# Performance work log

Hardware: AMD Instinct MI355X
Metric: run time of the kernel (lower is better)

Reference implementation:

```python
import jax, jax.numpy as jnp
import numpy as np

N, H_DIM, LATENT, MLP_H, F_OUT = 256, 128, 128, 256, 16
SUPP = 0.5  # ancestor_suppression_strength
EPS = 1e-12


def setup_inputs() -> dict:
    key = jax.random.key(0)
    ks = jax.random.split(key, 12)
    def w(k, shape):
        fan_in = shape[0]
        return jax.random.normal(k, shape, jnp.float32) / np.sqrt(fan_in)
    return {
        'z': jax.random.normal(ks[0], (LATENT,), jnp.float32),
        'targets': jax.random.randint(ks[1], (N, N), 0, 2, jnp.int32),
        'pos_emb': jax.random.normal(ks[2], (N, H_DIM), jnp.float32),
        'Ws1': w(ks[3], (H_DIM, H_DIM)),
        'Wn1': w(ks[4], (H_DIM, H_DIM)),
        'b1': jnp.zeros((H_DIM,), jnp.float32),
        'Ws2': w(ks[5], (H_DIM, H_DIM)),
        'Wn2': w(ks[6], (H_DIM, H_DIM)),
        'b2': jnp.zeros((H_DIM,), jnp.float32),
        'Wm1': w(ks[7], (LATENT + 3 * H_DIM, MLP_H)),
        'bm1': jnp.zeros((MLP_H,), jnp.float32),
        'Wm2': w(ks[8], (MLP_H, 1)),
        'bm2': jnp.zeros((1,), jnp.float32),
        'Wf': w(ks[9], (H_DIM, F_OUT)),
        'bf': jnp.zeros((F_OUT,), jnp.float32),
    }


def reference(z, targets, pos_emb, Ws1, Wn1, b1, Ws2, Wn2, b2,
              Wm1, bm1, Wm2, bm2, Wf, bf):
    tgt = jnp.tril(targets.astype(jnp.float32), -1)  # [N,N] strict lower: row=child, col=parent
    idx = jnp.arange(N)
    h0 = z  # decoder_init=None => hidden state init is z itself
    layers = ((Ws1, Wn1, b1), (Ws2, Wn2, b2))

    def gnn(Hs, M, active):
        # M[dst, src]: messages aggregated over incoming (parent) edges
        for Ws, Wn, b in layers:
            Hs = jax.nn.relu(Hs @ Ws + (M @ Hs) @ Wn + b) * active[:, None]
        return Hs

    def step(carry, t):
        Hs, anc, lp = carry
        Hs = Hs.at[t].set(h0 + pos_emb[t])          # new node t
        active = (idx <= t).astype(jnp.float32)
        M = tgt * (idx < t)[:, None].astype(jnp.float32)  # edges added in steps < t
        Hs = gnn(Hs, M, active)
        h_t = Hs[t]
        cand = (idx < t).astype(jnp.float32)        # candidate parents i < t
        mlp_in = jnp.concatenate([
            jnp.broadcast_to(h_t, (N, H_DIM)), Hs,
            jnp.broadcast_to(z, (N, LATENT)),
            jnp.broadcast_to(pos_emb[t], (N, H_DIM))], axis=1)
        logits = (jax.nn.relu(mlp_in @ Wm1 + bm1) @ Wm2 + bm2)[:, 0]
        probs = jax.nn.sigmoid(logits)
        # suppression[i] = prod_{j<t} (1 - s * anc[j][i])
        supp = jnp.prod(jnp.where((idx < t)[:, None], 1.0 - SUPP * anc, 1.0), axis=0)
        adj = probs * supp
        gt = tgt[t]
        logp = gt * jnp.log(adj + EPS) + (1.0 - gt) * jnp.log(1.0 - adj + EPS)
        lp = lp + jnp.sum(logp * cand)
        # ancestors of t = union over parents p of (anc[p] | {p})
        anc_t = jnp.minimum(1.0, gt @ anc + gt)
        anc = anc.at[t].set(anc_t)
        return (Hs, anc, lp), None

    H0 = jnp.zeros((N, H_DIM), jnp.float32).at[0].set(h0)
    anc0 = jnp.zeros((N, N), jnp.float32)
    (Hs, anc, lp), _ = jax.lax.scan(step, (H0, anc0, jnp.float32(0.0)), jnp.arange(1, N))
    # node_feature_decoder path: one more GNN pass over the full graph
    Hs = gnn(Hs, tgt, jnp.ones((N,), jnp.float32))
    X_out = Hs @ Wf + bf
    return tgt, X_out, lp
```

## Files before the change

### kernel.cpp

```cpp
#include <hip/hip_runtime.h>

#define NN 256
#define HD 128
#define GNN_NB 64
#define MLP_NB 64
#define NBLK 128
#define NTHR 512
#define D_HS 3
#define D_H1 2

#define HS_OFF 0
#define H1R_OFF 98304
#define PROG_OFF 163840
#define MF_OFF   (163840 + 2048)

#define STH_L 0
#define STM_L 512
#define PT_L  1024
#define TGT_L 0
#define PTM_L 2048
#define PT3_L 10240
#define HC_L  11264
#define CT_L  11776
#define CZ_L  12032
#define W2_L  12288
#define HP_L  12544
#define PART_L 12800
#define ANC_L 13312
#define LP_L  13344
#define LDS_FLOATS 13360

__device__ __forceinline__ float2 ldc_f2(const float* p) {
    unsigned long long u = __hip_atomic_load((const unsigned long long*)p,
                                             __ATOMIC_RELAXED, __HIP_MEMORY_SCOPE_AGENT);
    float2 r;
    r.x = __uint_as_float((unsigned)u);
    r.y = __uint_as_float((unsigned)(u >> 32));
    return r;
}
__device__ __forceinline__ void stc_f(float* p, float v) {
    __hip_atomic_store((unsigned*)p, __float_as_uint(v),
                       __ATOMIC_RELAXED, __HIP_MEMORY_SCOPE_AGENT);
}
__device__ __forceinline__ unsigned ldf(const unsigned* p) {
    return __hip_atomic_load(p, __ATOMIC_RELAXED, __HIP_MEMORY_SCOPE_AGENT);
}
__device__ __forceinline__ void stf(unsigned* p, unsigned v) {
    __hip_atomic_store(p, v, __ATOMIC_RELAXED, __HIP_MEMORY_SCOPE_AGENT);
}

__device__ __forceinline__ void bar_lds() {
    asm volatile("s_waitcnt lgkmcnt(0)\n\ts_barrier" ::: "memory");
}

__device__ __forceinline__ void wait_gnn(const unsigned* prog, const unsigned* mf,
                                         int b, unsigned dataTh, unsigned ringTh, int mlpTh)
{
    const int tid = threadIdx.x;
    if (tid < GNN_NB) {
        const unsigned th = (tid < b) ? dataTh : ringTh;
        if (th)
            while (ldf(prog + tid * 32) < th) __builtin_amdgcn_s_sleep(1);
    } else if (tid < 2 * GNN_NB) {
        if (mlpTh > 0)
            while ((int)ldf(mf + (tid - GNN_NB) * 32) < mlpTh) __builtin_amdgcn_s_sleep(1);
    }
    __syncthreads();
    asm volatile("" ::: "memory");
}

#define ISS(i) \
    float2 va##i, vb##i, vc##i, vd##i; \
    if ((i) < nst) { \
        const float* p_ = gsrc + (i) * 32 * HD; \
        if ((un >> (4 * (i)    )) & 1u) va##i = ldc_f2(p_); \
        if ((un >> (4 * (i) + 1)) & 1u) vb##i = ldc_f2(p_ + HD); \
        if ((un >> (4 * (i) + 2)) & 1u) vc##i = ldc_f2(p_ + 2 * HD); \
        if ((un >> (4 * (i) + 3)) & 1u) vd##i = ldc_f2(p_ + 3 * HD); \
    }
#define ACCP(v, b) { \
    const float f0_ = (float)((s0 >> (b)) & 1u); \
    const float f1_ = (float)((s1 >> (b)) & 1u); \
    const float f2_ = (float)((s2 >> (b)) & 1u); \
    const float f3_ = (float)((s3 >> (b)) & 1u); \
    m0.x = fmaf(f0_, v.x, m0.x); m0.y = fmaf(f0_, v.y, m0.y); \
    m1.x = fmaf(f1_, v.x, m1.x); m1.y = fmaf(f1_, v.y, m1.y); \
    m2.x = fmaf(f2_, v.x, m2.x); m2.y = fmaf(f2_, v.y, m2.y); \
    m3.x = fmaf(f3_, v.x, m3.x); m3.y = fmaf(f3_, v.y, m3.y); }
#define ACC1(v, b) if ((un >> (b)) & 1u) { ACCP(v, b) }
#define CNS(i) if ((i) < nst) { ACC1(va##i, 4*(i)) ACC1(vb##i, 4*(i)+1) \
                                ACC1(vc##i, 4*(i)+2) ACC1(vd##i, 4*(i)+3) }

__device__ __forceinline__ void layer(const float* src, float* dst, const float* bias,
    const float* z, const float* pos_emb, float* lds,
    const float2 (&wsA)[16], const float2 (&wnA)[16],
    unsigned mk0, unsigned mk1, unsigned mk2, unsigned mk3,
    int R0, int rmax, int tgate, int tnew, int lane, int wv, int tid)
{
    const int rmaxblk = min(rmax, R0 + 3);
    const int nst = (rmaxblk + 31) >> 5;
    const unsigned s0 = (R0     < tgate) ? mk0 : 0u;
    const unsigned s1 = (R0 + 1 < tgate) ? mk1 : 0u;
    const unsigned s2 = (R0 + 2 < tgate) ? mk2 : 0u;
    const unsigned s3 = (R0 + 3 < tgate) ? mk3 : 0u;
    const unsigned un = s0 | s1 | s2 | s3;

    if (tnew >= R0 && tnew < R0 + 4) {
        const int dr = tnew - R0;
        if (tid < HD) lds[STH_L + dr * HD + tid] = z[tid] + pos_emb[tnew * HD + tid];
    }

    const float* gsrc = src + wv * 4 * HD + 2 * lane;
    float2 m0 = make_float2(0.f, 0.f), m1 = m0, m2 = m0, m3 = m0;
    ISS(0) ISS(1) ISS(2) ISS(3) ISS(4) ISS(5) ISS(6) ISS(7)
    CNS(0) CNS(1) CNS(2) CNS(3) CNS(4) CNS(5) CNS(6) CNS(7)

    float* pt = lds + PT_L + (wv * 4) * HD + 2 * lane;
    *(float2*)pt = m0; *(float2*)(pt + HD) = m1;
    *(float2*)(pt + 2 * HD) = m2; *(float2*)(pt + 3 * HD) = m3;
    bar_lds();
    {
        const int dr = tid >> 7, k = tid & 127;
        float s = 0.f;
#pragma unroll
        for (int w = 0; w < 8; ++w) s += lds[PT_L + (w * 4 + dr) * HD + k];
        lds[STM_L + dr * HD + k] = s;
    }
    bar_lds();
    const int ks = wv * 16;
    float2 a0 = make_float2(0.f, 0.f), a1 = a0, a2 = a0, a3 = a0;
#define MV(dr, areg) { \
    const float4 hp = *(const float4*)(lds + STH_L + (dr) * HD + ks + 4 * kq); \
    const float4 mp = *(const float4*)(lds + STM_L + (dr) * HD + ks + 4 * kq); \
    areg.x = fmaf(hp.x, wsA[4*kq].x,   fmaf(mp.x, wnA[4*kq].x,   areg.x)); \
    areg.y = fmaf(hp.x, wsA[4*kq].y,   fmaf(mp.x, wnA[4*kq].y,   areg.y)); \
    areg.x = fmaf(hp.y, wsA[4*kq+1].x, fmaf(mp.y, wnA[4*kq+1].x, areg.x)); \
    areg.y = fmaf(hp.y, wsA[4*kq+1].y, fmaf(mp.y, wnA[4*kq+1].y, areg.y)); \
    areg.x = fmaf(hp.z, wsA[4*kq+2].x, fmaf(mp.z, wnA[4*kq+2].x, areg.x)); \
    areg.y = fmaf(hp.z, wsA[4*kq+2].y, fmaf(mp.z, wnA[4*kq+2].y, areg.y)); \
    areg.x = fmaf(hp.w, wsA[4*kq+3].x, fmaf(mp.w, wnA[4*kq+3].x, areg.x)); \
    areg.y = fmaf(hp.w, wsA[4*kq+3].y, fmaf(mp.w, wnA[4*kq+3].y, areg.y)); }
#pragma unroll
    for (int kq = 0; kq < 4; ++kq) { MV(0, a0) MV(1, a1) MV(2, a2) MV(3, a3) }
#undef MV
    *(float2*)pt = a0; *(float2*)(pt + HD) = a1;
    *(float2*)(pt + 2 * HD) = a2; *(float2*)(pt + 3 * HD) = a3;
    bar_lds();
    {
        const int dr = tid >> 7, c = tid & 127;
        float o = bias[c];
#pragma unroll
        for (int w = 0; w < 8; ++w) o += lds[PT_L + (w * 4 + dr) * HD + c];
        o = fmaxf(o, 0.f);
        lds[STH_L + dr * HD + c] = o;
        const int R = R0 + dr;
        if (R <= rmaxblk) stc_f(dst + R * HD + c, o);
    }
}

__device__ __forceinline__ void ct_calc(const float* hsP, const float* pos_emb,
                                        const float* Wm1, float* lds, int s)
{
    const int tid = threadIdx.x;
    if (tid < 64) {
        const float2 v = ldc_f2(hsP + s * HD + 2 * tid);
        lds[HP_L + 2 * tid] = v.x; lds[HP_L + 2 * tid + 1] = v.y;
    } else if (tid < 128) {
        const int l2 = tid - 64;
        lds[HP_L + 128 + 2 * l2]     = pos_emb[s * HD + 2 * l2];
        lds[HP_L + 128 + 2 * l2 + 1] = pos_emb[s * HD + 2 * l2 + 1];
    }
    __syncthreads();
    const int c = tid & 255, half = tid >> 8;
    float acc = 0.f;
    const float* w = half ? (Wm1 + 384 * 256 + c) : (Wm1 + c);
    const float* hh = lds + HP_L + half * 128;
#pragma unroll 4
    for (int k = 0; k < HD; ++k) acc = fmaf(hh[k], w[k * 256], acc);
    lds[PART_L + half * 256 + c] = acc;
    __syncthreads();
    if (tid < 256)
        lds[CT_L + tid] = lds[CZ_L + tid] + lds[PART_L + tid] + lds[PART_L + 256 + tid];
}

__device__ __forceinline__ void mlp_step(const float* hsP, const float* bm2,
                                         const float4 (&wm)[16], float* lds, int mb, int s)
{
    const int tid = threadIdx.x, lane = tid & 63, wv = tid >> 6;
    const int ks = wv * 16;
    if (wv < 4) {
        const int i = 4 * mb + wv;
        float2 v = make_float2(0.f, 0.f);
        if (i < s) v = ldc_f2(hsP + i * HD + 2 * lane);
        *(float2*)(lds + HC_L + wv * HD + 2 * lane) = v;
    }
    __syncthreads();
    float4 a0 = make_float4(0.f, 0.f, 0.f, 0.f), a1 = a0, a2 = a0, a3 = a0;
#pragma unroll
    for (int kk = 0; kk < 16; ++kk) {
        const int k = ks + kk;
        const float h0 = lds[HC_L + 0 * HD + k];
        const float h1 = lds[HC_L + 1 * HD + k];
        const float h2 = lds[HC_L + 2 * HD + k];
        const float h3 = lds[HC_L + 3 * HD + k];
        const float4 w = wm[kk];
        a0.x = fmaf(h0, w.x, a0.x); a0.y = fmaf(h0, w.y, a0.y);
        a0.z = fmaf(h0, w.z, a0.z); a0.w = fmaf(h0, w.w, a0.w);
        a1.x = fmaf(h1, w.x, a1.x); a1.y = fmaf(h1, w.y, a1.y);
        a1.z = fmaf(h1, w.z, a1.z); a1.w = fmaf(h1, w.w, a1.w);
        a2.x = fmaf(h2, w.x, a2.x); a2.y = fmaf(h2, w.y, a2.y);
        a2.z = fmaf(h2, w.z, a2.z); a2.w = fmaf(h2, w.w, a2.w);
        a3.x = fmaf(h3, w.x, a3.x); a3.y = fmaf(h3, w.y, a3.y);
        a3.z = fmaf(h3, w.z, a3.z); a3.w = fmaf(h3, w.w, a3.w);
    }
    *(float4*)(lds + PTM_L + (wv * 4 + 0) * 256 + 4 * lane) = a0;
    *(float4*)(lds + PTM_L + (wv * 4 + 1) * 256 + 4 * lane) = a1;
    *(float4*)(lds + PTM_L + (wv * 4 + 2) * 256 + 4 * lane) = a2;
    *(float4*)(lds + PTM_L + (wv * 4 + 3) * 256 + 4 * lane) = a3;
    __syncthreads();
    {
        const int c = tid & 255, ci2 = (tid >> 8) * 2;
#pragma unroll
        for (int q = 0; q < 2; ++q) {
            const int ci = ci2 + q;
            float v = lds[CT_L + c];
#pragma unroll
            for (int w = 0; w < 8; ++w) v += lds[PTM_L + (w * 4 + ci) * 256 + c];
            lds[PT3_L + ci * 256 + c] = fmaxf(v, 0.f) * lds[W2_L + c];
        }
    }
    __syncthreads();
    if (wv < 4) {
        const int ci = wv, i = 4 * mb + ci;
        if (i < s) {
            float sd = lds[PT3_L + ci * 256 + lane] + lds[PT3_L + ci * 256 + 64 + lane]
                     + lds[PT3_L + ci * 256 + 128 + lane] + lds[PT3_L + ci * 256 + 192 + lane];
#pragma unroll
            for (int off = 32; off > 0; off >>= 1) sd += __shfl_xor(sd, off);
            if (lane == 0) {
                const unsigned* gtl = (const unsigned*)(lds + TGT_L) + s * 8;
                unsigned* ancl = (unsigned*)(lds + ANC_L);
                const float logit = sd + bm2[0];
                const float prob = 1.f / (1.f + expf(-logit));
                unsigned cnt = 0, has = 0;
#pragma unroll
                for (int w = 0; w < 8; ++w) {
                    const unsigned av = ancl[ci * 8 + w];
                    cnt += __popc(av);
                    has |= av & gtl[w];
                }
                const float supp = ldexpf(1.f, -(int)cnt);
                const float adj = prob * supp;
                const unsigned gt = (gtl[i >> 5] >> (i & 31)) & 1u;
                const float lpv = gt ? logf(adj + 1e-12f) : logf(1.f - adj + 1e-12f);
                atomicAdd((float*)(lds + LP_L), lpv);
                if (has | gt) ancl[ci * 8 + (s >> 5)] |= (1u << (s & 31));
            }
        }
    }
}

extern "C" __global__ void __launch_bounds__(NTHR, 2)
fused_gnn(const float* z, const int* targets, const float* pos_emb,
          const float* Ws1, const float* Wn1, const float* b1,
          const float* Ws2, const float* Wn2, const float* b2,
          const float* Wm1, const float* bm1, const float* Wm2, const float* bm2,
          const float* Wf, const float* bf, float* out, float* ws)
{
    __shared__ __align__(16) float lds[LDS_FLOATS];
    const int b = blockIdx.x;
    const int tid = threadIdx.x, lane = tid & 63, wv = tid >> 6;

    unsigned* prog = (unsigned*)(ws + PROG_OFF);
    unsigned* mf   = (unsigned*)(ws + MF_OFF);
    float* lp_out = out + NN * NN + NN * 16;
    const int ks = wv * 16;

    if (b < GNN_NB) {
        const int R0 = b * 4;
        float2 ws1[16], wn1[16], ws2[16], wn2[16];
#pragma unroll
        for (int kk = 0; kk < 16; ++kk) {
            ws1[kk] = *(const float2*)(Ws1 + (ks + kk) * HD + 2 * lane);
            wn1[kk] = *(const float2*)(Wn1 + (ks + kk) * HD + 2 * lane);
            ws2[kk] = *(const float2*)(Ws2 + (ks + kk) * HD + 2 * lane);
            wn2[kk] = *(const float2*)(Wn2 + (ks + kk) * HD + 2 * lane);
        }
        unsigned mk0, mk1, mk2, mk3;
        {
            const int srcl = (lane < 32) ? (((lane >> 2) << 5) + wv * 4 + (lane & 3)) : 0;
#define BALLOT_MK(dr, dst) { \
            const int r_ = R0 + (dr); \
            const bool p_ = (lane < 32) && (srcl < r_) && (targets[r_ * NN + srcl] != 0); \
            const unsigned long long bm_ = __ballot(p_); \
            dst = (unsigned)__builtin_amdgcn_readfirstlane((int)(unsigned)bm_); }
            BALLOT_MK(0, mk0) BALLOT_MK(1, mk1) BALLOT_MK(2, mk2) BALLOT_MK(3, mk3)
#undef BALLOT_MK
        }
        lds[STH_L + tid] = (b == 0 && tid < HD) ? z[tid] : 0.f;
        {
            const int dr = tid >> 7, c = tid & 127, r = R0 + dr;
            stc_f(ws + HS_OFF + r * HD + c, (r == 0) ? z[c] : 0.f);
        }
        if (wv < 4) {
            const int r = R0 + wv;
            const int4 tv = ((const int4*)(targets + r * NN))[lane];
            float4 ov;
            ov.x = (4 * lane     < r) ? (float)tv.x : 0.f;
            ov.y = (4 * lane + 1 < r) ? (float)tv.y : 0.f;
            ov.z = (4 * lane + 2 < r) ? (float)tv.z : 0.f;
            ov.w = (4 * lane + 3 < r) ? (float)tv.w : 0.f;
            ((float4*)(out + r * NN))[lane] = ov;
        }
        __syncthreads();
        if (tid == 0) stf(prog + b * 32, 1u);

        for (int t = 1; t <= 256; ++t) {
            const float* hsP = ws + HS_OFF + ((t - 1) % D_HS) * 32768;
            float* h1c = ws + H1R_OFF + (t & 1) * 32768;
            float* hsN = ws + HS_OFF + (t % D_HS) * 32768;
            const int rmax  = (t <= 255) ? t : 255;
            const int tgate = (t <= 255) ? t : 300;
            const int tnew  = (t <= 255) ? t : -1;
            const bool act = (R0 <= rmax);

            if (act) {
                wait_gnn(prog, mf, b, 2u * t - 1u,
                         (t > D_H1) ? (2u * (t - D_H1) + 1u) : 0u, 0);
                layer(hsP, h1c, b1, z, pos_emb, lds, ws1, wn1,
                      mk0, mk1, mk2, mk3, R0, rmax, tgate, tnew, lane, wv, tid);
            }
            __syncthreads();
            if (tid == 0) stf(prog + b * 32, 2u * t);

            if (act) {
                wait_gnn(prog, mf, b, 2u * t,
                         (t > D_HS) ? (2u * (t - D_HS + 1)) : 0u, t - D_HS);
                layer(h1c, hsN, b2, z, pos_emb, lds, ws2, wn2,
                      mk0, mk1, mk2, mk3, R0, rmax, tgate, -1, lane, wv, tid);
            }
            __syncthreads();
            if (tid == 0) stf(prog + b * 32, 2u * t + 1u);
        }

        if (wv < 4) {
            const int r = R0 + wv;
            const float* strow = lds + STH_L + wv * HD;
            const int f = lane & 15, kp = lane >> 4;
            float sacc = 0.f;
#pragma unroll
            for (int k = 0; k < 32; ++k)
                sacc = fmaf(strow[kp * 32 + k], Wf[(kp * 32 + k) * 16 + f], sacc);
            sacc += __shfl_xor(sacc, 16);
            sacc += __shfl_xor(sacc, 32);
            if (lane < 16) out[NN * NN + r * 16 + f] = sacc + bf[f];
        }
    } else {
        const int mb = b - GNN_NB;
        float4 wm[16];
#pragma unroll
        for (int kk = 0; kk < 16; ++kk)
            wm[kk] = *(const float4*)(Wm1 + (128 + ks + kk) * 256 + 4 * lane);
        {
            unsigned* tg = (unsigned*)(lds + TGT_L);
            for (int rr = 0; rr < 32; ++rr) {
                const int r = wv * 32 + rr;
#pragma unroll
                for (int q = 0; q < 4; ++q) {
                    const int j = q * 64 + lane;
                    const unsigned long long bm = __ballot(j < r && targets[r * NN + j] != 0);
                    if (lane == 0) {
                        tg[r * 8 + 2 * q]     = (unsigned)bm;
                        tg[r * 8 + 2 * q + 1] = (unsigned)(bm >> 32);
                    }
                }
            }
        }
        if (tid < 256) {
            lds[W2_L + tid] = Wm2[tid];
            float acc = bm1[tid];
            for (int k = 0; k < HD; ++k) acc = fmaf(z[k], Wm1[(256 + k) * 256 + tid], acc);
            lds[CZ_L + tid] = acc;
        }
        if (tid < 32) ((unsigned*)(lds + ANC_L))[tid] = 0u;
        if (tid == 0) lds[LP_L] = 0.f;

        for (int s = 1; s <= 255; ++s) {
            if (tid < GNN_NB) {
                const unsigned need = 2u * (unsigned)s + 1u;
                while (ldf(prog + tid * 32) < need) __builtin_amdgcn_s_sleep(1);
            }
            __syncthreads();
            const float* hsP = ws + HS_OFF + (s % D_HS) * 32768;
            if (4 * mb < s) {
                ct_calc(hsP, pos_emb, Wm1, lds, s);
                __syncthreads();
                mlp_step(hsP, bm2, wm, lds, mb, s);
            }
            __syncthreads();
            if (tid == 0) stf(mf + mb * 32, (unsigned)s);
        }
        __syncthreads();
        if (tid == 0) atomicAdd(lp_out, lds[LP_L]);
    }
}

extern "C" void kernel_launch(void* const* d_in, const int* in_sizes, int n_in,
                              void* d_out, int out_size, void* d_ws, size_t ws_size,
                              hipStream_t stream)
{
    const float* z       = (const float*)d_in[0];
    const int*   targets = (const int*)d_in[1];
    const float* pos_emb = (const float*)d_in[2];
    const float* Ws1     = (const float*)d_in[3];
    const float* Wn1     = (const float*)d_in[4];
    const float* b1      = (const float*)d_in[5];
    const float* Ws2     = (const float*)d_in[6];
    const float* Wn2     = (const float*)d_in[7];
    const float* b2      = (const float*)d_in[8];
    const float* Wm1     = (const float*)d_in[9];
    const float* bm1     = (const float*)d_in[10];
    const float* Wm2     = (const float*)d_in[11];
    const float* bm2     = (const float*)d_in[12];
    const float* Wf      = (const float*)d_in[13];
    const float* bf      = (const float*)d_in[14];
    float* out = (float*)d_out;
    float* ws  = (float*)d_ws;

    (void)hipMemsetAsync(ws + PROG_OFF, 0, 2 * GNN_NB * 32 * sizeof(unsigned), stream);
    (void)hipMemsetAsync(out + NN * NN + NN * 16, 0, sizeof(float), stream);

    void* args[17] = {
        (void*)&z, (void*)&targets, (void*)&pos_emb,
        (void*)&Ws1, (void*)&Wn1, (void*)&b1,
        (void*)&Ws2, (void*)&Wn2, (void*)&b2,
        (void*)&Wm1, (void*)&bm1, (void*)&Wm2, (void*)&bm2,
        (void*)&Wf, (void*)&bf, (void*)&out, (void*)&ws
    };
    (void)hipLaunchCooperativeKernel((const void*)fused_gnn, dim3(NBLK), dim3(NTHR),
                                     args, 0, stream);
}
```

Baseline: 1.982 ms.

## Split GNN rows across twice as many blocks and fuse layer output reduction

Doubles the GNN block count so each block owns two rows instead of four, raising the grid to 192 cooperative blocks. The per-layer matvec is restructured so each thread holds 32 scalar weights for one output column over a k-slice and reduces with wave shuffles, replacing the LDS partial-sum pass and one barrier. The aim is to shorten the per-step critical path of the serial decode. In exchange there are more blocks polling progress flags, higher register pressure, and the occupancy hint in launch bounds is dropped.

```diff
diff --git a/kernel.cpp b/kernel.cpp
--- a/kernel.cpp
+++ b/kernel.cpp
@@ -2,9 +2,9 @@
 
 #define NN 256
 #define HD 128
-#define GNN_NB 64
+#define GNN_NB 128
 #define MLP_NB 64
-#define NBLK 128
+#define NBLK 192
 #define NTHR 512
 #define D_HS 3
 #define D_H1 2
@@ -12,11 +12,11 @@
 #define HS_OFF 0
 #define H1R_OFF 98304
 #define PROG_OFF 163840
-#define MF_OFF   (163840 + 2048)
+#define MF_OFF   (163840 + 4096)
 
 #define STH_L 0
-#define STM_L 512
-#define PT_L  1024
+#define STM_L 256
+#define PT_L  512
 #define TGT_L 0
 #define PTM_L 2048
 #define PT3_L 10240
@@ -61,7 +61,7 @@
         const unsigned th = (tid < b) ? dataTh : ringTh;
         if (th)
             while (ldf(prog + tid * 32) < th) __builtin_amdgcn_s_sleep(1);
-    } else if (tid < 2 * GNN_NB) {
+    } else if (tid < GNN_NB + MLP_NB) {
         if (mlpTh > 0)
             while ((int)ldf(mf + (tid - GNN_NB) * 32) < mlpTh) __builtin_amdgcn_s_sleep(1);
     }
@@ -81,81 +81,71 @@
 #define ACCP(v, b) { \
     const float f0_ = (float)((s0 >> (b)) & 1u); \
     const float f1_ = (float)((s1 >> (b)) & 1u); \
-    const float f2_ = (float)((s2 >> (b)) & 1u); \
-    const float f3_ = (float)((s3 >> (b)) & 1u); \
     m0.x = fmaf(f0_, v.x, m0.x); m0.y = fmaf(f0_, v.y, m0.y); \
-    m1.x = fmaf(f1_, v.x, m1.x); m1.y = fmaf(f1_, v.y, m1.y); \
-    m2.x = fmaf(f2_, v.x, m2.x); m2.y = fmaf(f2_, v.y, m2.y); \
-    m3.x = fmaf(f3_, v.x, m3.x); m3.y = fmaf(f3_, v.y, m3.y); }
+    m1.x = fmaf(f1_, v.x, m1.x); m1.y = fmaf(f1_, v.y, m1.y); }
 #define ACC1(v, b) if ((un >> (b)) & 1u) { ACCP(v, b) }
 #define CNS(i) if ((i) < nst) { ACC1(va##i, 4*(i)) ACC1(vb##i, 4*(i)+1) \
                                 ACC1(vc##i, 4*(i)+2) ACC1(vd##i, 4*(i)+3) }
 
-__device__ __forceinline__ void layer(const float* src, float* dst, const float* bias,
+__device__ __forceinline__ void layer(const float* src, float* dst, float bc,
     const float* z, const float* pos_emb, float* lds,
-    const float2 (&wsA)[16], const float2 (&wnA)[16],
-    unsigned mk0, unsigned mk1, unsigned mk2, unsigned mk3,
-    int R0, int rmax, int tgate, int tnew, int lane, int wv, int tid)
-{
-    const int rmaxblk = min(rmax, R0 + 3);
+    const float (&wsA)[32], const float (&wnA)[32],
+    unsigned mk0, unsigned mk1,
+    int R0, int rmax, int tgate, int tnew, int lane, int wv, int tid, int c, int kbase)
+{
+    const int rmaxblk = min(rmax, R0 + 1);
     const int nst = (rmaxblk + 31) >> 5;
     const unsigned s0 = (R0     < tgate) ? mk0 : 0u;
     const unsigned s1 = (R0 + 1 < tgate) ? mk1 : 0u;
-    const unsigned s2 = (R0 + 2 < tgate) ? mk2 : 0u;
-    const unsigned s3 = (R0 + 3 < tgate) ? mk3 : 0u;
-    const unsigned un = s0 | s1 | s2 | s3;
-
-    if (tnew >= R0 && tnew < R0 + 4) {
+    const unsigned un = s0 | s1;
+
+    if (tnew >= R0 && tnew < R0 + 2) {
         const int dr = tnew - R0;
         if (tid < HD) lds[STH_L + dr * HD + tid] = z[tid] + pos_emb[tnew * HD + tid];
     }
 
     const float* gsrc = src + wv * 4 * HD + 2 * lane;
-    float2 m0 = make_float2(0.f, 0.f), m1 = m0, m2 = m0, m3 = m0;
+    float2 m0 = make_float2(0.f, 0.f), m1 = m0;
     ISS(0) ISS(1) ISS(2) ISS(3) ISS(4) ISS(5) ISS(6) ISS(7)
     CNS(0) CNS(1) CNS(2) CNS(3) CNS(4) CNS(5) CNS(6) CNS(7)
 
-    float* pt = lds + PT_L + (wv * 4) * HD + 2 * lane;
-    *(float2*)pt = m0; *(float2*)(pt + HD) = m1;
-    *(float2*)(pt + 2 * HD) = m2; *(float2*)(pt + 3 * HD) = m3;
+    float* pt = lds + PT_L + (wv * 2) * HD + 2 * lane;
+    *(float2*)pt = m0;
+    *(float2*)(pt + HD) = m1;
     bar_lds();
-    {
+    if (tid < 256) {
         const int dr = tid >> 7, k = tid & 127;
         float s = 0.f;
 #pragma unroll
-        for (int w = 0; w < 8; ++w) s += lds[PT_L + (w * 4 + dr) * HD + k];
+        for (int w = 0; w < 8; ++w) s += lds[PT_L + (w * 2 + dr) * HD + k];
         lds[STM_L + dr * HD + k] = s;
     }
     bar_lds();
-    const int ks = wv * 16;
-    float2 a0 = make_float2(0.f, 0.f), a1 = a0, a2 = a0, a3 = a0;
-#define MV(dr, areg) { \
-    const float4 hp = *(const float4*)(lds + STH_L + (dr) * HD + ks + 4 * kq); \
-    const float4 mp = *(const float4*)(lds + STM_L + (dr) * HD + ks + 4 * kq); \
-    areg.x = fmaf(hp.x, wsA[4*kq].x,   fmaf(mp.x, wnA[4*kq].x,   areg.x)); \
-    areg.y = fmaf(hp.x, wsA[4*kq].y,   fmaf(mp.x, wnA[4*kq].y,   areg.y)); \
-    areg.x = fmaf(hp.y, wsA[4*kq+1].x, fmaf(mp.y, wnA[4*kq+1].x, areg.x)); \
-    areg.y = fmaf(hp.y, wsA[4*kq+1].y, fmaf(mp.y, wnA[4*kq+1].y, areg.y)); \
-    areg.x = fmaf(hp.z, wsA[4*kq+2].x, fmaf(mp.z, wnA[4*kq+2].x, areg.x)); \
-    areg.y = fmaf(hp.z, wsA[4*kq+2].y, fmaf(mp.z, wnA[4*kq+2].y, areg.y)); \
-    areg.x = fmaf(hp.w, wsA[4*kq+3].x, fmaf(mp.w, wnA[4*kq+3].x, areg.x)); \
-    areg.y = fmaf(hp.w, wsA[4*kq+3].y, fmaf(mp.w, wnA[4*kq+3].y, areg.y)); }
-#pragma unroll
-    for (int kq = 0; kq < 4; ++kq) { MV(0, a0) MV(1, a1) MV(2, a2) MV(3, a3) }
-#undef MV
-    *(float2*)pt = a0; *(float2*)(pt + HD) = a1;
-    *(float2*)(pt + 2 * HD) = a2; *(float2*)(pt + 3 * HD) = a3;
-    bar_lds();
-    {
-        const int dr = tid >> 7, c = tid & 127;
-        float o = bias[c];
-#pragma unroll
-        for (int w = 0; w < 8; ++w) o += lds[PT_L + (w * 4 + dr) * HD + c];
-        o = fmaxf(o, 0.f);
-        lds[STH_L + dr * HD + c] = o;
-        const int R = R0 + dr;
-        if (R <= rmaxblk) stc_f(dst + R * HD + c, o);
-    }
+    float acc0 = 0.f, acc1 = 0.f;
+#pragma unroll
+    for (int q = 0; q < 8; ++q) {
+        const float4 h0 = *(const float4*)(lds + STH_L + kbase + 4 * q);
+        const float4 mm0 = *(const float4*)(lds + STM_L + kbase + 4 * q);
+        const float4 h1 = *(const float4*)(lds + STH_L + HD + kbase + 4 * q);
+        const float4 mm1 = *(const float4*)(lds + STM_L + HD + kbase + 4 * q);
+        acc0 = fmaf(h0.x, wsA[4*q],   fmaf(mm0.x, wnA[4*q],   acc0));
+        acc0 = fmaf(h0.y, wsA[4*q+1], fmaf(mm0.y, wnA[4*q+1], acc0));
+        acc0 = fmaf(h0.z, wsA[4*q+2], fmaf(mm0.z, wnA[4*q+2], acc0));
+        acc0 = fmaf(h0.w, wsA[4*q+3], fmaf(mm0.w, wnA[4*q+3], acc0));
+        acc1 = fmaf(h1.x, wsA[4*q],   fmaf(mm1.x, wnA[4*q],   acc1));
+        acc1 = fmaf(h1.y, wsA[4*q+1], fmaf(mm1.y, wnA[4*q+1], acc1));
+        acc1 = fmaf(h1.z, wsA[4*q+2], fmaf(mm1.z, wnA[4*q+2], acc1));
+        acc1 = fmaf(h1.w, wsA[4*q+3], fmaf(mm1.w, wnA[4*q+3], acc1));
+    }
+    acc0 += __shfl_xor(acc0, 16); acc0 += __shfl_xor(acc0, 32);
+    acc1 += __shfl_xor(acc1, 16); acc1 += __shfl_xor(acc1, 32);
+    const float o0 = fmaxf(acc0 + bc, 0.f);
+    const float o1 = fmaxf(acc1 + bc, 0.f);
+    const int kg = lane >> 4;
+    if (kg == 0) { if (R0     <= rmaxblk) stc_f(dst + R0 * HD + c, o0); }
+    else if (kg == 1) { if (R0 + 1 <= rmaxblk) stc_f(dst + (R0 + 1) * HD + c, o1); }
+    else if (kg == 2) lds[STH_L + c] = o0;
+    else              lds[STH_L + HD + c] = o1;
 }
 
 __device__ __forceinline__ void ct_calc(const float* hsP, const float* pos_emb,
@@ -260,7 +250,7 @@
     }
 }
 
-extern "C" __global__ void __launch_bounds__(NTHR, 2)
+extern "C" __global__ void __launch_bounds__(NTHR)
 fused_gnn(const float* z, const int* targets, const float* pos_emb,
           const float* Ws1, const float* Wn1, const float* b1,
           const float* Ws2, const float* Wn2, const float* b2,
@@ -274,19 +264,21 @@
     unsigned* prog = (unsigned*)(ws + PROG_OFF);
     unsigned* mf   = (unsigned*)(ws + MF_OFF);
     float* lp_out = out + NN * NN + NN * 16;
-    const int ks = wv * 16;
 
     if (b < GNN_NB) {
-        const int R0 = b * 4;
-        float2 ws1[16], wn1[16], ws2[16], wn2[16];
-#pragma unroll
-        for (int kk = 0; kk < 16; ++kk) {
-            ws1[kk] = *(const float2*)(Ws1 + (ks + kk) * HD + 2 * lane);
-            wn1[kk] = *(const float2*)(Wn1 + (ks + kk) * HD + 2 * lane);
-            ws2[kk] = *(const float2*)(Ws2 + (ks + kk) * HD + 2 * lane);
-            wn2[kk] = *(const float2*)(Wn2 + (ks + kk) * HD + 2 * lane);
-        }
-        unsigned mk0, mk1, mk2, mk3;
+        const int R0 = b * 2;
+        const int c = 16 * wv + (lane & 15);
+        const int kbase = 32 * (lane >> 4);
+        float ws1[32], wn1[32], ws2[32], wn2[32];
+#pragma unroll
+        for (int i = 0; i < 32; ++i) {
+            ws1[i] = Ws1[(kbase + i) * HD + c];
+            wn1[i] = Wn1[(kbase + i) * HD + c];
+            ws2[i] = Ws2[(kbase + i) * HD + c];
+            wn2[i] = Wn2[(kbase + i) * HD + c];
+        }
+        const float b1c = b1[c], b2c = b2[c];
+        unsigned mk0, mk1;
         {
             const int srcl = (lane < 32) ? (((lane >> 2) << 5) + wv * 4 + (lane & 3)) : 0;
 #define BALLOT_MK(dr, dst) { \
@@ -294,15 +286,15 @@
             const bool p_ = (lane < 32) && (srcl < r_) && (targets[r_ * NN + srcl] != 0); \
             const unsigned long long bm_ = __ballot(p_); \
             dst = (unsigned)__builtin_amdgcn_readfirstlane((int)(unsigned)bm_); }
-            BALLOT_MK(0, mk0) BALLOT_MK(1, mk1) BALLOT_MK(2, mk2) BALLOT_MK(3, mk3)
+            BALLOT_MK(0, mk0) BALLOT_MK(1, mk1)
 #undef BALLOT_MK
         }
-        lds[STH_L + tid] = (b == 0 && tid < HD) ? z[tid] : 0.f;
-        {
-            const int dr = tid >> 7, c = tid & 127, r = R0 + dr;
-            stc_f(ws + HS_OFF + r * HD + c, (r == 0) ? z[c] : 0.f);
-        }
-        if (wv < 4) {
+        if (tid < 256) lds[STH_L + tid] = (b == 0 && tid < HD) ? z[tid] : 0.f;
+        if (tid < 256) {
+            const int dr = tid >> 7, cc = tid & 127, r = R0 + dr;
+            stc_f(ws + HS_OFF + r * HD + cc, (r == 0) ? z[cc] : 0.f);
+        }
+        if (wv < 2) {
             const int r = R0 + wv;
             const int4 tv = ((const int4*)(targets + r * NN))[lane];
             float4 ov;
@@ -327,8 +319,8 @@
             if (act) {
                 wait_gnn(prog, mf, b, 2u * t - 1u,
                          (t > D_H1) ? (2u * (t - D_H1) + 1u) : 0u, 0);
-                layer(hsP, h1c, b1, z, pos_emb, lds, ws1, wn1,
-                      mk0, mk1, mk2, mk3, R0, rmax, tgate, tnew, lane, wv, tid);
+                layer(hsP, h1c, b1c, z, pos_emb, lds, ws1, wn1,
+                      mk0, mk1, R0, rmax, tgate, tnew, lane, wv, tid, c, kbase);
             }
             __syncthreads();
             if (tid == 0) stf(prog + b * 32, 2u * t);
@@ -336,14 +328,14 @@
             if (act) {
                 wait_gnn(prog, mf, b, 2u * t,
                          (t > D_HS) ? (2u * (t - D_HS + 1)) : 0u, t - D_HS);
-                layer(h1c, hsN, b2, z, pos_emb, lds, ws2, wn2,
-                      mk0, mk1, mk2, mk3, R0, rmax, tgate, -1, lane, wv, tid);
+                layer(h1c, hsN, b2c, z, pos_emb, lds, ws2, wn2,
+                      mk0, mk1, R0, rmax, tgate, -1, lane, wv, tid, c, kbase);
             }
             __syncthreads();
             if (tid == 0) stf(prog + b * 32, 2u * t + 1u);
         }
 
-        if (wv < 4) {
+        if (wv < 2) {
             const int r = R0 + wv;
             const float* strow = lds + STH_L + wv * HD;
             const int f = lane & 15, kp = lane >> 4;
@@ -357,6 +349,7 @@
         }
     } else {
         const int mb = b - GNN_NB;
+        const int ks = wv * 16;
         float4 wm[16];
 #pragma unroll
         for (int kk = 0; kk < 16; ++kk)
@@ -427,7 +420,7 @@
     float* out = (float*)d_out;
     float* ws  = (float*)d_ws;
 
-    (void)hipMemsetAsync(ws + PROG_OFF, 0, 2 * GNN_NB * 32 * sizeof(unsigned), stream);
+    (void)hipMemsetAsync(ws + PROG_OFF, 0, (GNN_NB + MLP_NB) * 32 * sizeof(unsigned), stream);
     (void)hipMemsetAsync(out + NN * NN + NN * 16, 0, sizeof(float), stream);
 
     void* args[17] = {
```

After: 1.869 ms. 1.06x faster.
